# Performance work log

Hardware: AMD Instinct MI355X
Metric: run time of the kernel (lower is better)

The kernel has to match this reference:

```python
import jax, jax.numpy as jnp
import numpy as np

B, N, D, F_IN, F_OUT, MAX_DEG = 256, 512, 6, 128, 128, 6


def setup_inputs() -> dict:
    key = jax.random.key(0)
    k_atoms, k_deg, k_idx, k_w, k_b = jax.random.split(key, 5)
    atoms = jax.random.normal(k_atoms, (B, N, F_IN), dtype=jnp.float32)
    # structured edges: per-atom degree in [0, MAX_DEG-1], valid neighbor ids in
    # the first `deg` slots, -1 padding afterwards (NGFP convention)
    deg = jax.random.randint(k_deg, (B, N, 1), 0, MAX_DEG)
    nbr = jax.random.randint(k_idx, (B, N, D), 0, N)
    slot = jnp.arange(D)[None, None, :]
    edges = jnp.where(slot < deg, nbr, -1).astype(jnp.int64)
    W = jax.random.normal(k_w, (MAX_DEG, F_IN, F_OUT), dtype=jnp.float32) * (1.0 / np.sqrt(F_IN))
    b = jax.random.normal(k_b, (MAX_DEG, F_OUT), dtype=jnp.float32) * 0.01
    return {"atoms": atoms, "edges": edges, "W": W, "b": b}


def reference(atoms, edges, W, b):
    # lookup_neighbors with include_self=True: gather neighbor rows (-1 -> zero row)
    atoms_p = jnp.pad(atoms, ((0, 0), (1, 0), (0, 0)))          # [B, N+1, F]; row 0 is zeros
    gathered = jax.vmap(lambda a, e: a[e])(atoms_p, edges + 1)  # [B, N, D, F]
    summed = gathered.sum(axis=-2) + atoms                      # [B, N, F] (self included)
    degrees = (edges != -1).sum(axis=-1, keepdims=True)         # [B, N, 1]
    out = jnp.zeros(summed.shape[:-1] + (W.shape[-1],), dtype=summed.dtype)
    for d in range(MAX_DEG):
        h = jax.nn.relu(summed @ W[d] + b[d])                   # [B, N, F_OUT]
        out = out + h * (degrees == d).astype(summed.dtype)
    return out
```

## Files before the change

### kernel.cpp

```cpp
#include <hip/hip_runtime.h>


typedef short bf16x8 __attribute__((ext_vector_type(8)));
typedef float f32x4  __attribute__((ext_vector_type(4)));
typedef unsigned short ushort_t;
typedef unsigned int uint_t;

constexpr int Nn = 512;
constexpr int Ff = 128;
constexpr int BN = 256 * 512;
constexpr int ROWSTRIDE = 34;

constexpr size_t WS_GC     = 0;
constexpr size_t WS_REGION = 256;
constexpr size_t WS_WT     = 256 + (size_t)6 * BN * 4;
constexpr size_t WS_SUMMED = WS_WT + 196608;
constexpr size_t WS_NEEDED = WS_SUMMED + (size_t)BN * 128 * 2;

__device__ inline ushort_t f2bf(float f) {
    uint_t u = __float_as_uint(f);
    return (ushort_t)((u + 0x7FFFu + ((u >> 16) & 1u)) >> 16);
}

__device__ inline bool detect_is64(const int* edges32) {
    int probe = edges32[2 * (threadIdx.x & 63) + 1];
    return __any(probe > 0) == 0;
}

__global__ __launch_bounds__(256, 2)
void k1_pre(const float* __restrict__ atoms,
            const int*   __restrict__ edges32,
            const float* __restrict__ W,
            int* __restrict__ gcnt,
            int* __restrict__ region,
            ushort_t* __restrict__ Wt,
            ushort_t* __restrict__ summed) {
    const int tid   = threadIdx.x;
    const int mol   = blockIdx.x >> 2;
    const int slice = blockIdx.x & 3;
    const bool is64 = detect_is64(edges32);

    __shared__ float    Arows[Nn * ROWSTRIDE];
    __shared__ ushort_t nbp[Nn * 6];
    __shared__ int      hist[6], base_sh[6];

    if (blockIdx.x < 384) {
        int linear = blockIdx.x * 256 + tid;
        int d = linear >> 14, rem = linear & 16383;
        int k = rem >> 7, n = rem & 127;
        Wt[d * 16384 + n * 128 + k] = f2bf(W[linear]);
    }

    {
        const size_t ebase = (size_t)mol * (Nn * 6);
        for (int i = tid; i < Nn * 6; i += 256) {
            int e = is64 ? edges32[(ebase + i) * 2] : edges32[ebase + i];
            nbp[i] = (ushort_t)(e >= 0 ? e : 0xFFFF);
        }
    }

    {
        const float4* gsrc = (const float4*)(atoms + (size_t)mol * (Nn * Ff) + slice * 32);
        #pragma unroll
        for (int it = 0; it < 16; it++) {
            int idx = tid + it * 256;
            int row = idx >> 3, q = idx & 7;
            float4 v = gsrc[row * 32 + q];
            int la = row * ROWSTRIDE + q * 4;
            float2 p0; p0.x = v.x; p0.y = v.y;
            float2 p1; p1.x = v.z; p1.y = v.w;
            *(float2*)&Arows[la]     = p0;
            *(float2*)&Arows[la + 2] = p1;
        }
    }
    __syncthreads();

    if (slice == 0) {
        if (tid < 6) hist[tid] = 0;
        __syncthreads();
        int dg[2], rk[2];
        #pragma unroll
        for (int s = 0; s < 2; s++) {
            int row = tid + s * 256;
            int dd = 0;
            #pragma unroll
            for (int j = 0; j < 6; j++) dd += (nbp[row * 6 + j] != 0xFFFF) ? 1 : 0;
            dg[s] = dd;
            rk[s] = atomicAdd(&hist[dd], 1);
        }
        __syncthreads();
        if (tid < 6) base_sh[tid] = atomicAdd(&gcnt[tid], hist[tid]);
        __syncthreads();
        #pragma unroll
        for (int s = 0; s < 2; s++)
            region[dg[s] * BN + base_sh[dg[s]] + rk[s]] = mol * Nn + tid + s * 256;
    }

    const int h = tid & 3, cbase = h * 8;
    #pragma unroll
    for (int rd = 0; rd < 8; rd++) {
        const int row = rd * 64 + (tid >> 2);
        float2 acc[4];
        #pragma unroll
        for (int c = 0; c < 4; c++)
            acc[c] = *(const float2*)&Arows[row * ROWSTRIDE + cbase + 2 * c];
        #pragma unroll
        for (int j = 0; j < 6; j++) {
            int e = nbp[row * 6 + j];
            if (e != 0xFFFF) {
                const float* src = &Arows[e * ROWSTRIDE + cbase];
                #pragma unroll
                for (int c = 0; c < 4; c++) {
                    float2 v = *(const float2*)&src[2 * c];
                    acc[c].x += v.x; acc[c].y += v.y;
                }
            }
        }
        uint4 o;
        o.x = (uint_t)f2bf(acc[0].x) | ((uint_t)f2bf(acc[0].y) << 16);
        o.y = (uint_t)f2bf(acc[1].x) | ((uint_t)f2bf(acc[1].y) << 16);
        o.z = (uint_t)f2bf(acc[2].x) | ((uint_t)f2bf(acc[2].y) << 16);
        o.w = (uint_t)f2bf(acc[3].x) | ((uint_t)f2bf(acc[3].y) << 16);
        *(uint4*)(summed + (size_t)(mol * Nn + row) * Ff + slice * 32 + cbase) = o;
    }
}

__global__ __launch_bounds__(256, 4)
void k2_gemm(const ushort_t* __restrict__ summed,
             const float*    __restrict__ bias,
             const ushort_t* __restrict__ Wt,
             const int*      __restrict__ region,
             const int*      __restrict__ gcnt,
             float*          __restrict__ out) {
    int cnts[6];
    #pragma unroll
    for (int dd = 0; dd < 6; dd++) cnts[dd] = gcnt[dd];
    const int bid = blockIdx.x;
    int d = -1, t = 0, accum = 0;
    #pragma unroll
    for (int dd = 0; dd < 6; dd++) {
        int tl = (cnts[dd] + 127) >> 7;
        if (d < 0 && bid < accum + tl) { d = dd; t = bid - accum; }
        accum += tl;
    }
    if (d < 0) return;
    const int count = cnts[d];
    const int m0 = t * 128;
    const int nrows = min(128, count - m0);

    __shared__ __attribute__((aligned(16))) ushort_t Bsh[128 * 136];
    __shared__ int ids[128];

    const int tid = threadIdx.x;
    if (tid < 128) {
        int idx = m0 + tid;
        if (idx >= count) idx = count - 1;
        ids[tid] = region[d * BN + idx];
    }
    {
        const uint4* Wg = (const uint4*)(Wt + (size_t)d * 16384);
        #pragma unroll
        for (int i = 0; i < 8; i++) {
            int idx = tid + i * 256;
            int n = idx >> 4, c = idx & 15;
            *(uint4*)&Bsh[n * 136 + c * 8] = Wg[idx];
        }
    }
    __syncthreads();

    const int lane = tid & 63, w = tid >> 6;
    const int mrow = w * 32;
    const int kq = lane >> 4;
    const int ml = lane & 15;

    bf16x8 af[2][4];
    #pragma unroll
    for (int mt = 0; mt < 2; mt++) {
        const int row = ids[mrow + mt * 16 + ml];
        const bf16x8* sp = (const bf16x8*)(summed + (size_t)row * Ff + kq * 8);
        #pragma unroll
        for (int k0 = 0; k0 < 4; k0++) af[mt][k0] = sp[k0 * 4];
    }

    #pragma unroll
    for (int nt = 0; nt < 8; nt++) {
        bf16x8 bfr[4];
        #pragma unroll
        for (int k0 = 0; k0 < 4; k0++)
            bfr[k0] = *(const bf16x8*)&Bsh[(nt * 16 + ml) * 136 + k0 * 32 + kq * 8];
        f32x4 c0 = {0.f, 0.f, 0.f, 0.f}, c1 = {0.f, 0.f, 0.f, 0.f};
        #pragma unroll
        for (int k0 = 0; k0 < 4; k0++) {
            c0 = __builtin_amdgcn_mfma_f32_16x16x32_bf16(af[0][k0], bfr[k0], c0, 0, 0, 0);
            c1 = __builtin_amdgcn_mfma_f32_16x16x32_bf16(af[1][k0], bfr[k0], c1, 0, 0, 0);
        }
        const int col = nt * 16 + ml;
        const float bcol = bias[d * Ff + col];
        #pragma unroll
        for (int mt = 0; mt < 2; mt++) {
            f32x4 cc = mt ? c1 : c0;
            #pragma unroll
            for (int reg = 0; reg < 4; reg++) {
                int rl = mrow + mt * 16 + kq * 4 + reg;
                if (rl < nrows) {
                    float v = cc[reg] + bcol;
                    out[(size_t)ids[rl] * Ff + col] = v > 0.f ? v : 0.f;
                }
            }
        }
    }
}

__global__ __launch_bounds__(128, 2)
void graphconv_fallback(const float* __restrict__ atoms,
                        const int* __restrict__ edges_raw,
                        const float* __restrict__ W,
                        const float* __restrict__ bias,
                        float* __restrict__ out) {
    const int tid = threadIdx.x;
    const int d = blockIdx.x % 6;
    const int k = blockIdx.x / 6;
    const int a0 = k * 256;
    __shared__ int eds[256 * 6];
    __shared__ int list[256];
    __shared__ int cnt;
    __shared__ float sv[2][Ff];
    bool is64;
    { int v = edges_raw[2 * (tid & 63) + 1]; is64 = (__ballot(v > 0) == 0ull); }
    if (!is64) { for (int i = tid; i < 256 * 6; i += 128) eds[i] = edges_raw[a0 * 6 + i]; }
    else       { for (int i = tid; i < 256 * 6; i += 128) eds[i] = edges_raw[2 * (a0 * 6 + i)]; }
    if (tid == 0) cnt = 0;
    __syncthreads();
    for (int i = tid; i < 256; i += 128) {
        int deg = 0;
        #pragma unroll
        for (int j = 0; j < 6; j++) deg += (eds[i * 6 + j] != -1) ? 1 : 0;
        if (deg == d) { int p = atomicAdd(&cnt, 1); list[p] = i; }
    }
    float Wreg[Ff];
    { const float* Wd = W + (size_t)d * Ff * Ff;
      #pragma unroll
      for (int f = 0; f < Ff; f++) Wreg[f] = Wd[f * Ff + tid]; }
    const float breg = bias[d * Ff + tid];
    __syncthreads();
    const int n = cnt;
    const float* batch_atoms = atoms + (size_t)(a0 / Nn) * Nn * Ff;
    const int row0 = a0 % Nn;
    for (int ii = 0; ii < n; ii++) {
        const int i = list[ii];
        float s = batch_atoms[(row0 + i) * Ff + tid];
        #pragma unroll
        for (int j = 0; j < 6; j++) {
            int e = eds[i * 6 + j];
            if (e != -1) s += batch_atoms[e * Ff + tid];
        }
        float* buf = sv[ii & 1];
        buf[tid] = s;
        __syncthreads();
        float acc = breg;
        const float4* sv4 = (const float4*)buf;
        #pragma unroll
        for (int fc = 0; fc < Ff / 4; fc++) {
            float4 x = sv4[fc];
            acc = fmaf(x.x, Wreg[4 * fc + 0], acc);
            acc = fmaf(x.y, Wreg[4 * fc + 1], acc);
            acc = fmaf(x.z, Wreg[4 * fc + 2], acc);
            acc = fmaf(x.w, Wreg[4 * fc + 3], acc);
        }
        out[(size_t)(a0 + i) * Ff + tid] = fmaxf(acc, 0.0f);
    }
}

extern "C" void kernel_launch(void* const* d_in, const int* in_sizes, int n_in,
                              void* d_out, int out_size, void* d_ws, size_t ws_size,
                              hipStream_t stream) {
    const float* atoms = (const float*)d_in[0];
    const int*   edges = (const int*)d_in[1];
    const float* W     = (const float*)d_in[2];
    const float* bias  = (const float*)d_in[3];
    float*       outp  = (float*)d_out;

    if (ws_size >= WS_NEEDED) {
        char* ws = (char*)d_ws;
        int*      gcnt   = (int*)(ws + WS_GC);
        int*      region = (int*)(ws + WS_REGION);
        ushort_t* Wt     = (ushort_t*)(ws + WS_WT);
        ushort_t* summed = (ushort_t*)(ws + WS_SUMMED);

        hipMemsetAsync(gcnt, 0, 32, stream);
        k1_pre<<<1024, 256, 0, stream>>>(atoms, edges, W, gcnt, region, Wt, summed);
        k2_gemm<<<1030, 256, 0, stream>>>(summed, bias, Wt, region, gcnt, outp);
    } else {
        graphconv_fallback<<<3072, 128, 0, stream>>>(atoms, edges, W, bias, outp);
    }
}
```

Before: 164.6 us.

## Halve k1 feature slices and transpose MFMA operands for vectorized output stores

The pre-pass kernel now splits each molecule into 8 feature slices of 16 floats instead of 4 slices of 32. This halves shared memory per block and raises the occupancy hint from 2 to 3, at the cost of reloading edges and neighbor lists twice as often. The GEMM swaps its MFMA operands so each lane holds 4 consecutive output columns of one row. It then writes bias+ReLU results as float4 stores instead of scattered scalar stores. The per-row output offsets are hoisted out of the tile loop.

```diff
diff --git a/kernel.cpp b/kernel.cpp
--- a/kernel.cpp
+++ b/kernel.cpp
@@ -9,7 +9,7 @@
 constexpr int Nn = 512;
 constexpr int Ff = 128;
 constexpr int BN = 256 * 512;
-constexpr int ROWSTRIDE = 34;
+constexpr int RS = 18;
 
 constexpr size_t WS_GC     = 0;
 constexpr size_t WS_REGION = 256;
@@ -27,7 +27,7 @@
     return __any(probe > 0) == 0;
 }
 
-__global__ __launch_bounds__(256, 2)
+__global__ __launch_bounds__(256, 3)
 void k1_pre(const float* __restrict__ atoms,
             const int*   __restrict__ edges32,
             const float* __restrict__ W,
@@ -36,11 +36,11 @@
             ushort_t* __restrict__ Wt,
             ushort_t* __restrict__ summed) {
     const int tid   = threadIdx.x;
-    const int mol   = blockIdx.x >> 2;
-    const int slice = blockIdx.x & 3;
+    const int mol   = blockIdx.x >> 3;
+    const int slice = blockIdx.x & 7;
     const bool is64 = detect_is64(edges32);
 
-    __shared__ float    Arows[Nn * ROWSTRIDE];
+    __shared__ float    Arows[Nn * RS];
     __shared__ ushort_t nbp[Nn * 6];
     __shared__ int      hist[6], base_sh[6];
 
@@ -53,20 +53,22 @@
 
     {
         const size_t ebase = (size_t)mol * (Nn * 6);
-        for (int i = tid; i < Nn * 6; i += 256) {
+        #pragma unroll
+        for (int it = 0; it < 12; it++) {
+            int i = tid + it * 256;
             int e = is64 ? edges32[(ebase + i) * 2] : edges32[ebase + i];
             nbp[i] = (ushort_t)(e >= 0 ? e : 0xFFFF);
         }
     }
 
     {
-        const float4* gsrc = (const float4*)(atoms + (size_t)mol * (Nn * Ff) + slice * 32);
-        #pragma unroll
-        for (int it = 0; it < 16; it++) {
+        const float4* gsrc = (const float4*)(atoms + (size_t)mol * (Nn * Ff) + slice * 16);
+        #pragma unroll
+        for (int it = 0; it < 8; it++) {
             int idx = tid + it * 256;
-            int row = idx >> 3, q = idx & 7;
+            int row = idx >> 2, q = idx & 3;
             float4 v = gsrc[row * 32 + q];
-            int la = row * ROWSTRIDE + q * 4;
+            int la = row * RS + q * 4;
             float2 p0; p0.x = v.x; p0.y = v.y;
             float2 p1; p1.x = v.z; p1.y = v.w;
             *(float2*)&Arows[la]     = p0;
@@ -96,19 +98,19 @@
             region[dg[s] * BN + base_sh[dg[s]] + rk[s]] = mol * Nn + tid + s * 256;
     }
 
-    const int h = tid & 3, cbase = h * 8;
-    #pragma unroll
-    for (int rd = 0; rd < 8; rd++) {
-        const int row = rd * 64 + (tid >> 2);
+    const int h = tid & 1, cbase = h * 8;
+    #pragma unroll
+    for (int rd = 0; rd < 4; rd++) {
+        const int row = rd * 128 + (tid >> 1);
         float2 acc[4];
         #pragma unroll
         for (int c = 0; c < 4; c++)
-            acc[c] = *(const float2*)&Arows[row * ROWSTRIDE + cbase + 2 * c];
+            acc[c] = *(const float2*)&Arows[row * RS + cbase + 2 * c];
         #pragma unroll
         for (int j = 0; j < 6; j++) {
             int e = nbp[row * 6 + j];
             if (e != 0xFFFF) {
-                const float* src = &Arows[e * ROWSTRIDE + cbase];
+                const float* src = &Arows[e * RS + cbase];
                 #pragma unroll
                 for (int c = 0; c < 4; c++) {
                     float2 v = *(const float2*)&src[2 * c];
@@ -121,7 +123,7 @@
         o.y = (uint_t)f2bf(acc[1].x) | ((uint_t)f2bf(acc[1].y) << 16);
         o.z = (uint_t)f2bf(acc[2].x) | ((uint_t)f2bf(acc[2].y) << 16);
         o.w = (uint_t)f2bf(acc[3].x) | ((uint_t)f2bf(acc[3].y) << 16);
-        *(uint4*)(summed + (size_t)(mol * Nn + row) * Ff + slice * 32 + cbase) = o;
+        *(uint4*)(summed + (size_t)(mol * Nn + row) * Ff + slice * 16 + cbase) = o;
     }
 }
 
@@ -169,45 +171,44 @@
     __syncthreads();
 
     const int lane = tid & 63, w = tid >> 6;
-    const int mrow = w * 32;
+    const int arow0 = w * 32;
     const int kq = lane >> 4;
     const int ml = lane & 15;
 
     bf16x8 af[2][4];
     #pragma unroll
     for (int mt = 0; mt < 2; mt++) {
-        const int row = ids[mrow + mt * 16 + ml];
+        const int row = ids[arow0 + mt * 16 + ml];
         const bf16x8* sp = (const bf16x8*)(summed + (size_t)row * Ff + kq * 8);
         #pragma unroll
         for (int k0 = 0; k0 < 4; k0++) af[mt][k0] = sp[k0 * 4];
     }
+    const bool v0 = (arow0 + ml) < nrows;
+    const bool v1 = (arow0 + 16 + ml) < nrows;
+    const int o0 = v0 ? (int)((size_t)ids[arow0 + ml] * Ff) : 0;
+    const int o1 = v1 ? (int)((size_t)ids[arow0 + 16 + ml] * Ff) : 0;
 
     #pragma unroll
     for (int nt = 0; nt < 8; nt++) {
-        bf16x8 bfr[4];
+        bf16x8 wfr[4];
         #pragma unroll
         for (int k0 = 0; k0 < 4; k0++)
-            bfr[k0] = *(const bf16x8*)&Bsh[(nt * 16 + ml) * 136 + k0 * 32 + kq * 8];
+            wfr[k0] = *(const bf16x8*)&Bsh[(nt * 16 + ml) * 136 + k0 * 32 + kq * 8];
         f32x4 c0 = {0.f, 0.f, 0.f, 0.f}, c1 = {0.f, 0.f, 0.f, 0.f};
         #pragma unroll
         for (int k0 = 0; k0 < 4; k0++) {
-            c0 = __builtin_amdgcn_mfma_f32_16x16x32_bf16(af[0][k0], bfr[k0], c0, 0, 0, 0);
-            c1 = __builtin_amdgcn_mfma_f32_16x16x32_bf16(af[1][k0], bfr[k0], c1, 0, 0, 0);
-        }
-        const int col = nt * 16 + ml;
-        const float bcol = bias[d * Ff + col];
-        #pragma unroll
-        for (int mt = 0; mt < 2; mt++) {
-            f32x4 cc = mt ? c1 : c0;
-            #pragma unroll
-            for (int reg = 0; reg < 4; reg++) {
-                int rl = mrow + mt * 16 + kq * 4 + reg;
-                if (rl < nrows) {
-                    float v = cc[reg] + bcol;
-                    out[(size_t)ids[rl] * Ff + col] = v > 0.f ? v : 0.f;
-                }
-            }
-        }
+            c0 = __builtin_amdgcn_mfma_f32_16x16x32_bf16(wfr[k0], af[0][k0], c0, 0, 0, 0);
+            c1 = __builtin_amdgcn_mfma_f32_16x16x32_bf16(wfr[k0], af[1][k0], c1, 0, 0, 0);
+        }
+        const int colb = nt * 16 + kq * 4;
+        const float4 bv = *(const float4*)&bias[d * Ff + colb];
+        float4 r0, r1;
+        r0.x = fmaxf(c0[0] + bv.x, 0.f); r0.y = fmaxf(c0[1] + bv.y, 0.f);
+        r0.z = fmaxf(c0[2] + bv.z, 0.f); r0.w = fmaxf(c0[3] + bv.w, 0.f);
+        r1.x = fmaxf(c1[0] + bv.x, 0.f); r1.y = fmaxf(c1[1] + bv.y, 0.f);
+        r1.z = fmaxf(c1[2] + bv.z, 0.f); r1.w = fmaxf(c1[3] + bv.w, 0.f);
+        if (v0) *(float4*)&out[o0 + colb] = r0;
+        if (v1) *(float4*)&out[o1 + colb] = r1;
     }
 }
 
@@ -288,7 +289,7 @@
         ushort_t* summed = (ushort_t*)(ws + WS_SUMMED);
 
         hipMemsetAsync(gcnt, 0, 32, stream);
-        k1_pre<<<1024, 256, 0, stream>>>(atoms, edges, W, gcnt, region, Wt, summed);
+        k1_pre<<<2048, 256, 0, stream>>>(atoms, edges, W, gcnt, region, Wt, summed);
         k2_gemm<<<1030, 256, 0, stream>>>(summed, bias, Wt, region, gcnt, outp);
     } else {
         graphconv_fallback<<<3072, 128, 0, stream>>>(atoms, edges, W, bias, outp);
```

Measured after the change: 167.0 us. No clear change (+1.4%).
